# Optimization experiments

Hardware: AMD Instinct MI355X
Metric: run time of the kernel (lower is better)

The kernel has to match this reference:

```python
import jax, jax.numpy as jnp
import numpy as np

T = 500        # num_target
R = 50         # num_resource
NS = 1000      # hard-coded sample count in the torch loop
F_STATE = 2    # raw state features; num_feature = F_STATE + T = 502
NOISE_F = 2
H1, H2 = 32, 16
NEG_SLOPE = 0.2


def _lrelu(x):
    return jnp.where(x >= 0, x, NEG_SLOPE * x)


def setup_inputs() -> dict:
    key = jax.random.key(0)
    ks = jax.random.split(key, 16)
    d = {}
    d["state"] = jax.random.normal(ks[0], (1, T, F_STATE), jnp.float32)
    d["def_cur_loc"] = jax.random.uniform(ks[1], (R, T), jnp.float32)
    d["feat_noise"] = jax.random.uniform(ks[2], (1, T, NOISE_F), jnp.float32)
    d["gumbel_u"] = jax.random.uniform(ks[3], (NS, R, T), jnp.float32, 1e-6, 1.0 - 1e-6)
    # learned / fixed parameters
    d["payoff"] = jax.random.normal(ks[4], (T, T), jnp.float32)
    # row-normalized adjacency surrogate
    a = jax.random.uniform(ks[5], (T, T), jnp.float32)
    d["norm_adj"] = a / jnp.sum(a, axis=1, keepdims=True)
    fin = F_STATE + T + NOISE_F  # 504 = num_feature + noise_feat
    d["gc1_w"] = jax.random.normal(ks[6], (fin, H1), jnp.float32) / np.sqrt(fin)
    d["gc1_b"] = jnp.zeros((H1,), jnp.float32)
    d["gc2_w"] = jax.random.normal(ks[7], (H1, H2), jnp.float32) / np.sqrt(H1)
    d["gc2_b"] = jnp.zeros((H2,), jnp.float32)
    d["bn_gamma"] = jnp.ones((T,), jnp.float32)
    d["bn_beta"] = jnp.zeros((T,), jnp.float32)
    d["actgen_w"] = jax.random.normal(ks[8], (H2 * T, T), jnp.float32) / np.sqrt(H2 * T)
    d["actgen_v"] = jax.random.normal(ks[9], (T, T), jnp.float32) / np.sqrt(T)
    return d


def reference(state, def_cur_loc, feat_noise, gumbel_u, payoff, norm_adj,
              gc1_w, gc1_b, gc2_w, gc2_b, bn_gamma, bn_beta,
              actgen_w, actgen_v):
    # x = cat(state, payoff, noise) -> (1, T, 504)
    x = jnp.concatenate([state, payoff[None], feat_noise], axis=2)

    def gcn(h, w, b):  # GraphConvolution: norm_adj @ (h @ w) + b
        return jnp.einsum('tu,buc->btc', norm_adj, h @ w) + b

    def bn(h):  # BatchNorm1d(T) in eval mode (running mean 0, var 1)
        return h * bn_gamma[None, :, None] + bn_beta[None, :, None]

    h = _lrelu(bn(gcn(x, gc1_w, gc1_b)))          # (1, T, 32); dropout is eval-mode identity
    h = _lrelu(bn(gcn(h, gc2_w, gc2_b)))          # (1, T, 16)
    xf = h.reshape(H2 * T)                        # x.view(-1, 16*T).squeeze()

    # act_gen: shared linear head + location projection -> per-resource logits (R, T)
    logits = xf @ actgen_w + def_cur_loc @ actgen_v

    # 1000 independent stochastic samples (the torch for-loop, fully batched):
    g = -jnp.log(-jnp.log(gumbel_u))              # (NS, R, T) gumbel noise
    act_estimates = jax.nn.softmax(logits[None] + g, axis=-1)  # (1000, R, T)
    # state_value head exists in the module but is not returned; omitted.
    return act_estimates
```

## Files before the change

kernel.cpp:

```cpp
#include <hip/hip_runtime.h>

#define T_ 500
#define R_ 50
#define NS_ 1000
#define H1_ 32
#define H2_ 16
#define NEG_ 0.2f

__device__ __forceinline__ float lrelu(float x) { return x >= 0.f ? x : NEG_ * x; }

__global__ __launch_bounds__(256) void k1_xw(const float* __restrict__ state,
                                             const float* __restrict__ payoff,
                                             const float* __restrict__ noise,
                                             const float* __restrict__ w,
                                             float* __restrict__ y1) {
    __shared__ float xs[504];
    __shared__ float red[8][H1_];
    int t = blockIdx.x, tid = threadIdx.x;
    for (int u = tid; u < T_; u += 256) xs[2 + u] = payoff[t * T_ + u];
    if (tid == 0) {
        xs[0] = state[t * 2];     xs[1] = state[t * 2 + 1];
        xs[502] = noise[t * 2];   xs[503] = noise[t * 2 + 1];
    }
    __syncthreads();
    int c = tid & 31, kg = tid >> 5;
    float acc = 0.f;
#pragma unroll 7
    for (int f = kg; f < 504; f += 8) acc += xs[f] * w[f * H1_ + c];
    red[kg][c] = acc;
    __syncthreads();
    if (tid < H1_) {
        float a = 0.f;
#pragma unroll
        for (int s = 0; s < 8; ++s) a += red[s][tid];
        y1[t * H1_ + tid] = a;
    }
}

__global__ __launch_bounds__(256) void k2_adj_fused(const float* __restrict__ adj,
                                                    const float* __restrict__ y1,
                                                    const float* __restrict__ b,
                                                    const float* __restrict__ gamma,
                                                    const float* __restrict__ beta,
                                                    const float* __restrict__ w2,
                                                    float* __restrict__ y2) {
    __shared__ float arow[T_];
    __shared__ float red[8][H1_];
    __shared__ float h1row[H1_];
    int t = blockIdx.x, tid = threadIdx.x;
    for (int u = tid; u < T_; u += 256) arow[u] = adj[t * T_ + u];
    __syncthreads();
    int c = tid & 31, kg = tid >> 5;
    float acc = 0.f;
#pragma unroll 4
    for (int u = kg; u < T_; u += 8) acc += arow[u] * y1[u * H1_ + c];
    red[kg][c] = acc;
    __syncthreads();
    if (tid < H1_) {
        float a = 0.f;
#pragma unroll
        for (int s = 0; s < 8; ++s) a += red[s][tid];
        h1row[tid] = lrelu((a + b[tid]) * gamma[t] + beta[t]);
    }
    __syncthreads();
    if (tid < H2_) {
        float a = 0.f;
#pragma unroll
        for (int cc = 0; cc < H1_; ++cc) a += h1row[cc] * w2[cc * H2_ + tid];
        y2[t * H2_ + tid] = a;
    }
}

__global__ __launch_bounds__(256) void k3_adj2_aw(const float* __restrict__ adj,
                                                  const float* __restrict__ y2,
                                                  const float* __restrict__ b2,
                                                  const float* __restrict__ gamma,
                                                  const float* __restrict__ beta,
                                                  const float* __restrict__ aw,
                                                  float* __restrict__ part1) {
    __shared__ float arow[T_];
    __shared__ float red[16][H2_];
    __shared__ float xfr[H2_];
    int t = blockIdx.x, tid = threadIdx.x;
    for (int u = tid; u < T_; u += 256) arow[u] = adj[t * T_ + u];
    __syncthreads();
    int c2 = tid & 15, kg = tid >> 4;
    float acc = 0.f;
#pragma unroll 4
    for (int u = kg; u < T_; u += 16) acc += arow[u] * y2[u * H2_ + c2];
    red[kg][c2] = acc;
    __syncthreads();
    if (tid < H2_) {
        float a = 0.f;
#pragma unroll
        for (int s = 0; s < 16; ++s) a += red[s][tid];
        xfr[tid] = lrelu((a + b2[tid]) * gamma[t] + beta[t]);
    }
    __syncthreads();
    float acc0 = 0.f, acc1 = 0.f;
#pragma unroll
    for (int c = 0; c < H2_; ++c) {
        float xv = xfr[c];
        const float* awr = aw + (t * H2_ + c) * T_;
        acc0 += xv * awr[tid];
        if (tid < T_ - 256) acc1 += xv * awr[256 + tid];
    }
    part1[t * T_ + tid] = acc0;
    if (tid < T_ - 256) part1[t * T_ + 256 + tid] = acc1;
}

__global__ __launch_bounds__(256) void k4_logits_part(const float* __restrict__ dloc,
                                                      const float* __restrict__ av,
                                                      const float* __restrict__ part1,
                                                      float* __restrict__ part2) {
    int r = blockIdx.x;
    int jb = blockIdx.y & 1, q = blockIdx.y >> 1;
    __shared__ float drow[125];
    int tid = threadIdx.x;
    int t0 = q * 125;
    if (tid < 125) drow[tid] = dloc[r * T_ + t0 + tid];
    __syncthreads();
    if (tid >= 250) return;
    int j = jb * 250 + tid;
    float acc = 0.f;
#pragma unroll 5
    for (int i = 0; i < 125; ++i) {
        int t = t0 + i;
        acc += drow[i] * av[t * T_ + j] + part1[t * T_ + j];
    }
    part2[q * (R_ * T_) + r * T_ + j] = acc;
}

__global__ __launch_bounds__(256) void k4_reduce(const float* __restrict__ part2,
                                                 float* __restrict__ logits) {
    int gid = blockIdx.x * 256 + threadIdx.x;
    if (gid >= R_ * T_) return;
    logits[gid] = part2[gid] + part2[R_ * T_ + gid] +
                  part2[2 * R_ * T_ + gid] + part2[3 * R_ * T_ + gid];
}

__global__ __launch_bounds__(256) void k7_softmax(const float4* __restrict__ gu,
                                                  const float4* __restrict__ logits,
                                                  float4* __restrict__ out) {
    int wave = threadIdx.x >> 6;
    int lane = threadIdx.x & 63;
    int row = blockIdx.x * 4 + wave;
    int r = row % R_;
    const float4* grow = gu + row * 125;
    const float4* lrow = logits + r * 125;
    bool has1 = lane < 61;

    float v[8];
    float4 g0 = grow[lane];
    float4 l0 = lrow[lane];
    v[0] = l0.x - __logf(-__logf(g0.x));
    v[1] = l0.y - __logf(-__logf(g0.y));
    v[2] = l0.z - __logf(-__logf(g0.z));
    v[3] = l0.w - __logf(-__logf(g0.w));
    if (has1) {
        float4 g1 = grow[64 + lane];
        float4 l1 = lrow[64 + lane];
        v[4] = l1.x - __logf(-__logf(g1.x));
        v[5] = l1.y - __logf(-__logf(g1.y));
        v[6] = l1.z - __logf(-__logf(g1.z));
        v[7] = l1.w - __logf(-__logf(g1.w));
    } else {
        v[4] = v[5] = v[6] = v[7] = -1e30f;
    }
    float m = fmaxf(fmaxf(fmaxf(v[0], v[1]), fmaxf(v[2], v[3])),
                    fmaxf(fmaxf(v[4], v[5]), fmaxf(v[6], v[7])));
#pragma unroll
    for (int off = 32; off > 0; off >>= 1) m = fmaxf(m, __shfl_xor(m, off));

    float ssum = 0.f;
#pragma unroll
    for (int i = 0; i < 8; ++i) {
        v[i] = (i < 4 || has1) ? __expf(v[i] - m) : 0.f;
        ssum += v[i];
    }
#pragma unroll
    for (int off = 32; off > 0; off >>= 1) ssum += __shfl_xor(ssum, off);
    float inv = 1.f / ssum;

    float4* orow = out + row * 125;
    float4 o0 = {v[0] * inv, v[1] * inv, v[2] * inv, v[3] * inv};
    orow[lane] = o0;
    if (has1) {
        float4 o1 = {v[4] * inv, v[5] * inv, v[6] * inv, v[7] * inv};
        orow[64 + lane] = o1;
    }
}

extern "C" void kernel_launch(void* const* d_in, const int* in_sizes, int n_in,
                              void* d_out, int out_size, void* d_ws, size_t ws_size,
                              hipStream_t stream) {
    const float* state  = (const float*)d_in[0];
    const float* dloc   = (const float*)d_in[1];
    const float* noise  = (const float*)d_in[2];
    const float* gu     = (const float*)d_in[3];
    const float* payoff = (const float*)d_in[4];
    const float* adj    = (const float*)d_in[5];
    const float* g1w    = (const float*)d_in[6];
    const float* g1b    = (const float*)d_in[7];
    const float* g2w    = (const float*)d_in[8];
    const float* g2b    = (const float*)d_in[9];
    const float* gamma  = (const float*)d_in[10];
    const float* beta   = (const float*)d_in[11];
    const float* aw     = (const float*)d_in[12];
    const float* av     = (const float*)d_in[13];
    float* out = (float*)d_out;

    float* ws     = (float*)d_ws;
    float* y1     = ws;
    float* y2     = ws + 16000;
    float* part1  = ws + 24000;
    float* part2  = ws + 274000;
    float* logits = ws + 374000;

    k1_xw<<<T_, 256, 0, stream>>>(state, payoff, noise, g1w, y1);
    k2_adj_fused<<<T_, 256, 0, stream>>>(adj, y1, g1b, gamma, beta, g2w, y2);
    k3_adj2_aw<<<T_, 256, 0, stream>>>(adj, y2, g2b, gamma, beta, aw, part1);
    k4_logits_part<<<dim3(R_, 8), 256, 0, stream>>>(dloc, av, part1, part2);
    k4_reduce<<<(R_ * T_ + 255) / 256, 256, 0, stream>>>(part2, logits);
    k7_softmax<<<(NS_ * R_) / 4, 256, 0, stream>>>(
        (const float4*)gu, (const float4*)logits, (float4*)out);
}
```

Baseline: 73.53 us.

## Rewrite Gumbel softmax as exp(logit) over -log2(u), dropping max reduction

Uses the identity exp(l - log(-log u)) = exp(l) / (-log u). The exponential of the logits is precomputed once per (resource, target) in the reduce kernel, so the per-sample softmax needs one log2 and one reciprocal per element. The ln-to-log2 constant cancels in normalization, which also removes the max-subtraction wave reduction. Output stores are made nontemporal. The cost is that without max subtraction exp(logit) can overflow or underflow when logits are large in magnitude.

After: 71.84 us. 2.3% less time.

```diff
diff --git a/kernel.cpp b/kernel.cpp
--- a/kernel.cpp
+++ b/kernel.cpp
@@ -6,6 +6,8 @@
 #define H1_ 32
 #define H2_ 16
 #define NEG_ 0.2f
+
+typedef float vf4 __attribute__((ext_vector_type(4)));
 
 __device__ __forceinline__ float lrelu(float x) { return x >= 0.f ? x : NEG_ * x; }
 
@@ -131,63 +133,57 @@
     part2[q * (R_ * T_) + r * T_ + j] = acc;
 }
 
-__global__ __launch_bounds__(256) void k4_reduce(const float* __restrict__ part2,
-                                                 float* __restrict__ logits) {
+__global__ __launch_bounds__(256) void k4_reduce_exp(const float* __restrict__ part2,
+                                                     float* __restrict__ elog) {
     int gid = blockIdx.x * 256 + threadIdx.x;
     if (gid >= R_ * T_) return;
-    logits[gid] = part2[gid] + part2[R_ * T_ + gid] +
-                  part2[2 * R_ * T_ + gid] + part2[3 * R_ * T_ + gid];
+    float v = part2[gid] + part2[R_ * T_ + gid] +
+              part2[2 * R_ * T_ + gid] + part2[3 * R_ * T_ + gid];
+    elog[gid] = __expf(v);
 }
 
 __global__ __launch_bounds__(256) void k7_softmax(const float4* __restrict__ gu,
-                                                  const float4* __restrict__ logits,
-                                                  float4* __restrict__ out) {
+                                                  const float4* __restrict__ elog,
+                                                  float* __restrict__ out) {
     int wave = threadIdx.x >> 6;
     int lane = threadIdx.x & 63;
     int row = blockIdx.x * 4 + wave;
     int r = row % R_;
     const float4* grow = gu + row * 125;
-    const float4* lrow = logits + r * 125;
+    const float4* erow = elog + r * 125;
     bool has1 = lane < 61;
 
-    float v[8];
     float4 g0 = grow[lane];
-    float4 l0 = lrow[lane];
-    v[0] = l0.x - __logf(-__logf(g0.x));
-    v[1] = l0.y - __logf(-__logf(g0.y));
-    v[2] = l0.z - __logf(-__logf(g0.z));
-    v[3] = l0.w - __logf(-__logf(g0.w));
+    float4 e0 = erow[lane];
+    float4 g1, e1;
     if (has1) {
-        float4 g1 = grow[64 + lane];
-        float4 l1 = lrow[64 + lane];
-        v[4] = l1.x - __logf(-__logf(g1.x));
-        v[5] = l1.y - __logf(-__logf(g1.y));
-        v[6] = l1.z - __logf(-__logf(g1.z));
-        v[7] = l1.w - __logf(-__logf(g1.w));
+        g1 = grow[64 + lane];
+        e1 = erow[64 + lane];
+    }
+    float p[8];
+    p[0] = e0.x * __builtin_amdgcn_rcpf(-__log2f(g0.x));
+    p[1] = e0.y * __builtin_amdgcn_rcpf(-__log2f(g0.y));
+    p[2] = e0.z * __builtin_amdgcn_rcpf(-__log2f(g0.z));
+    p[3] = e0.w * __builtin_amdgcn_rcpf(-__log2f(g0.w));
+    if (has1) {
+        p[4] = e1.x * __builtin_amdgcn_rcpf(-__log2f(g1.x));
+        p[5] = e1.y * __builtin_amdgcn_rcpf(-__log2f(g1.y));
+        p[6] = e1.z * __builtin_amdgcn_rcpf(-__log2f(g1.z));
+        p[7] = e1.w * __builtin_amdgcn_rcpf(-__log2f(g1.w));
     } else {
-        v[4] = v[5] = v[6] = v[7] = -1e30f;
-    }
-    float m = fmaxf(fmaxf(fmaxf(v[0], v[1]), fmaxf(v[2], v[3])),
-                    fmaxf(fmaxf(v[4], v[5]), fmaxf(v[6], v[7])));
-#pragma unroll
-    for (int off = 32; off > 0; off >>= 1) m = fmaxf(m, __shfl_xor(m, off));
-
-    float ssum = 0.f;
-#pragma unroll
-    for (int i = 0; i < 8; ++i) {
-        v[i] = (i < 4 || has1) ? __expf(v[i] - m) : 0.f;
-        ssum += v[i];
-    }
-#pragma unroll
-    for (int off = 32; off > 0; off >>= 1) ssum += __shfl_xor(ssum, off);
-    float inv = 1.f / ssum;
-
-    float4* orow = out + row * 125;
-    float4 o0 = {v[0] * inv, v[1] * inv, v[2] * inv, v[3] * inv};
-    orow[lane] = o0;
+        p[4] = p[5] = p[6] = p[7] = 0.f;
+    }
+    float s = ((p[0] + p[1]) + (p[2] + p[3])) + ((p[4] + p[5]) + (p[6] + p[7]));
+#pragma unroll
+    for (int off = 32; off > 0; off >>= 1) s += __shfl_xor(s, off);
+    float inv = __builtin_amdgcn_rcpf(s);
+
+    vf4* orow = (vf4*)(out + row * T_);
+    vf4 o0 = {p[0] * inv, p[1] * inv, p[2] * inv, p[3] * inv};
+    __builtin_nontemporal_store(o0, orow + lane);
     if (has1) {
-        float4 o1 = {v[4] * inv, v[5] * inv, v[6] * inv, v[7] * inv};
-        orow[64 + lane] = o1;
+        vf4 o1 = {p[4] * inv, p[5] * inv, p[6] * inv, p[7] * inv};
+        __builtin_nontemporal_store(o1, orow + 64 + lane);
     }
 }
 
@@ -215,13 +211,13 @@
     float* y2     = ws + 16000;
     float* part1  = ws + 24000;
     float* part2  = ws + 274000;
-    float* logits = ws + 374000;
+    float* elog   = ws + 374000;
 
     k1_xw<<<T_, 256, 0, stream>>>(state, payoff, noise, g1w, y1);
     k2_adj_fused<<<T_, 256, 0, stream>>>(adj, y1, g1b, gamma, beta, g2w, y2);
     k3_adj2_aw<<<T_, 256, 0, stream>>>(adj, y2, g2b, gamma, beta, aw, part1);
     k4_logits_part<<<dim3(R_, 8), 256, 0, stream>>>(dloc, av, part1, part2);
-    k4_reduce<<<(R_ * T_ + 255) / 256, 256, 0, stream>>>(part2, logits);
+    k4_reduce_exp<<<(R_ * T_ + 255) / 256, 256, 0, stream>>>(part2, elog);
     k7_softmax<<<(NS_ * R_) / 4, 256, 0, stream>>>(
-        (const float4*)gu, (const float4*)logits, (float4*)out);
-}
+        (const float4*)gu, (const float4*)elog, (float*)out);
+}
```
